# Kernel tuning notes

Measured on AMD Instinct MI355X. Metric: run time of the kernel, lower is better.

## Reference

```python
import jax, jax.numpy as jnp
import numpy as np

# FermiNet-style ansatz (Ansatz_fb) constants
N_U, N_D = 10, 10
N_E = N_U + N_D          # 20 electrons
N_A = 4                  # atoms
N_DET = 16
N_FB = 3
N_SV, N_PV = 256, 32
N_SV_OUT = 3 * N_SV + 2 * N_PV   # 832
N_B = 2048               # MCMC walkers (batch)
N_S_IN = 4 * N_A         # 16
N_P_IN = 4
D0 = 3 * N_S_IN + 2 * N_P_IN     # 56, input dim of first single-stream layer


def _lin(key, fan_in, shape):
    lim = 1.0 / np.sqrt(fan_in)
    return jax.random.uniform(key, shape, jnp.float32, -lim, lim)


def setup_inputs() -> dict:
    key = jax.random.key(0)
    ks = jax.random.split(key, 20)
    a = jnp.array([[0.0, 0.0, 0.0], [0.0, 0.0, 2.0], [2.0, 0.0, 0.0], [0.0, 2.0, 0.0]], jnp.float32)
    return {
        "r": jax.random.normal(ks[0], (N_B, N_E, 3), jnp.float32),
        "a": a,
        # single-stream layers: layer0 (D0->N_SV) then N_FB residual layers (N_SV_OUT->N_SV)
        "s_w0": _lin(ks[1], D0, (D0, N_SV)), "s_b0": _lin(ks[2], D0, (N_SV,)),
        "s_w": _lin(ks[3], N_SV_OUT, (N_FB, N_SV_OUT, N_SV)), "s_b": _lin(ks[4], N_SV_OUT, (N_FB, N_SV)),
        # pair-stream layers: layer0 (4->N_PV) then N_FB residual layers (N_PV->N_PV)
        "p_w0": _lin(ks[5], N_P_IN, (N_P_IN, N_PV)), "p_b0": _lin(ks[6], N_P_IN, (N_PV,)),
        "p_w": _lin(ks[7], N_PV, (N_FB, N_PV, N_PV)), "p_b": _lin(ks[8], N_PV, (N_FB, N_PV)),
        "vu_w": _lin(ks[9], N_SV_OUT, (N_SV_OUT, N_SV)), "vu_b": _lin(ks[10], N_SV_OUT, (N_SV,)),
        "vd_w": _lin(ks[11], N_SV_OUT, (N_SV_OUT, N_SV)), "vd_b": _lin(ks[12], N_SV_OUT, (N_SV,)),
        "wu_w": _lin(ks[13], N_SV, (N_SV, N_U * N_DET)), "wu_b": _lin(ks[14], N_SV, (N_U * N_DET,)),
        "wd_w": _lin(ks[15], N_SV, (N_SV, N_D * N_DET)), "wd_b": _lin(ks[16], N_SV, (N_D * N_DET,)),
        "wf_w": _lin(ks[17], N_DET, (N_DET, 1)),
    }


def fb_block(s_v, p_v):
    # s_v: [b, n_e, ds]; p_v: [b, n_e, n_e, dp]
    m_u = jnp.broadcast_to(s_v[:, :N_U].mean(1, keepdims=True), s_v.shape)  # tile mean over electrons
    m_d = jnp.broadcast_to(s_v[:, N_U:].mean(1, keepdims=True), s_v.shape)
    p_u = p_v[:, :N_U].mean(1)  # [b, n_e, dp]
    p_d = p_v[:, N_U:].mean(1)
    return jnp.concatenate([s_v, m_u, m_d, p_u, p_d], -1)


def reference(r, a, s_w0, s_b0, s_w, s_b, p_w0, p_b0, p_w, p_b, vu_w, vu_b, vd_w, vd_b, wu_w, wu_b, wd_w, wd_b, wf_w):
    n_b = r.shape[0]
    ra = r[:, :, None, :] - a[None, None]                      # [b, n_e, n_a, 3]
    ra_len = jnp.linalg.norm(ra, axis=-1, keepdims=True)
    rr = r[:, None, :, :] - r[:, :, None, :]                   # [b, n_e, n_e, 3]
    eye = jnp.eye(N_E, dtype=r.dtype)[None, :, :, None]
    rr_len = jnp.linalg.norm(rr + eye, axis=-1, keepdims=True)  # avoid 0 on diagonal
    s_v = jnp.concatenate([ra, ra_len], -1).reshape(n_b, N_E, -1)  # [b, n_e, 4*n_a]
    p_v = jnp.concatenate([rr, rr_len], -1)                        # [b, n_e, n_e, 4]

    blk = fb_block(s_v, p_v)
    s_v = jnp.tanh(blk @ s_w0 + s_b0)          # layer 0: no residual
    p_v = jnp.tanh(p_v @ p_w0 + p_b0)
    blk = fb_block(s_v, p_v)
    for i in range(N_FB):                       # residual layers
        s_v = jnp.tanh(blk @ s_w[i] + s_b[i]) + s_v
        p_v = jnp.tanh(p_v @ p_w[i] + p_b[i]) + p_v
        blk = fb_block(s_v, p_v)

    s_u = jnp.tanh(blk[:, :N_U] @ vu_w + vu_b)  # [b, n_u, n_sv]
    s_d = jnp.tanh(blk[:, N_U:] @ vd_w + vd_b)
    # chunk(n_det, dim=-1) then cat on new dim 1 == reshape+transpose
    w_u = (s_u @ wu_w + wu_b).reshape(n_b, N_U, N_DET, N_U).transpose(0, 2, 1, 3)  # [b, det, n_u, n_u]
    w_d = (s_d @ wd_w + wd_b).reshape(n_b, N_D, N_DET, N_D).transpose(0, 2, 1, 3)

    exp_u = jnp.exp(-jnp.linalg.norm(ra[:, :N_U], axis=-1)).sum(-1)  # [b, n_u]
    exp_d = jnp.exp(-jnp.linalg.norm(ra[:, N_U:], axis=-1)).sum(-1)
    orb_u = w_u * exp_u[:, None, :, None]
    orb_d = w_d * exp_d[:, None, :, None]

    # n_u, n_d > 1 -> det_one_e == 1, use slogdet path
    s_u_sgn, l_u = jnp.linalg.slogdet(orb_u)
    s_d_sgn, l_d = jnp.linalg.slogdet(orb_d)
    logdet = l_u + l_d                                       # [b, n_det]
    maxlogdet = jnp.max(logdet, axis=-1, keepdims=True)       # n_det > 1
    det = (s_u_sgn * s_d_sgn) * jnp.exp(logdet - maxlogdet)
    psi_ish = (det @ wf_w)[..., 0]                            # [b]
    log_psi = jnp.log(jnp.abs(psi_ish)) + maxlogdet[..., 0]
    return log_psi
```

## Files before the change

kernel.cpp:

```cpp
#include <hip/hip_runtime.h>
#include <math.h>


namespace {

constexpr float SQRT3 = 1.7320508075688772f;

__global__ __launch_bounds__(256, 2) void ansatz_fused(
    const float* __restrict__ r,
    const float* __restrict__ a_g,
    const float* __restrict__ s_w0,
    const float* __restrict__ s_b0,
    const float* __restrict__ s_w,
    const float* __restrict__ s_b,
    const float* __restrict__ p_w0,
    const float* __restrict__ p_b0,
    const float* __restrict__ p_w,
    const float* __restrict__ p_b,
    const float* __restrict__ vu_w, const float* __restrict__ vu_b,
    const float* __restrict__ vd_w, const float* __restrict__ vd_b,
    const float* __restrict__ wu_w, const float* __restrict__ wu_b,
    const float* __restrict__ wd_w, const float* __restrict__ wd_b,
    const float* __restrict__ wf_w,
    float* __restrict__ out)
{
  const int b = blockIdx.x;
  const int tid = threadIdx.x;

  __shared__ float svT[256 * 20];
  __shared__ float pvbuf[20 * 20 * 32];
  __shared__ float mu[256], md[256];
  __shared__ float puT[32 * 20], pdT[32 * 20];
  __shared__ float sinT[16 * 20];
  __shared__ float rl[20][3];
  __shared__ float apos[4][3];
  __shared__ float expv[20];
  __shared__ float lu_s[32], sg_s[32];

  if (tid < 60) (&rl[0][0])[tid] = r[b * 60 + tid];
  if (tid >= 64 && tid < 76) (&apos[0][0])[tid - 64] = a_g[tid - 64];
  __syncthreads();

  for (int t = tid; t < 320; t += 256) {
    int k = t / 20, e = t % 20;
    int at = k >> 2, comp = k & 3;
    float dx = rl[e][0] - apos[at][0];
    float dy = rl[e][1] - apos[at][1];
    float dz = rl[e][2] - apos[at][2];
    float v;
    if (comp == 0) v = dx;
    else if (comp == 1) v = dy;
    else if (comp == 2) v = dz;
    else v = sqrtf(dx * dx + dy * dy + dz * dz);
    sinT[k * 20 + e] = v;
  }
  for (int t = tid; t < 160; t += 256) {
    int half = t / 80, rem = t % 80, c = rem / 20, j = rem % 20;
    float s = 0.f;
    for (int i = half * 10; i < half * 10 + 10; ++i) {
      if (c < 3) {
        s += rl[j][c] - rl[i][c];
      } else if (i == j) {
        s += SQRT3;
      } else {
        float dx = rl[j][0] - rl[i][0], dy = rl[j][1] - rl[i][1], dz = rl[j][2] - rl[i][2];
        s += sqrtf(dx * dx + dy * dy + dz * dz);
      }
    }
    (half ? pdT : puT)[c * 20 + j] = s * 0.1f;
  }
  __syncthreads();

  if (tid < 20) {
    float s = 0.f;
    for (int at = 0; at < 4; ++at) s += expf(-sinT[(at * 4 + 3) * 20 + tid]);
    expv[tid] = s;
  }
  if (tid < 32) {
    int k = tid & 15, half = tid >> 4;
    float s = 0.f;
    for (int e = half * 10; e < half * 10 + 10; ++e) s += sinT[k * 20 + e];
    (half ? md : mu)[k] = s * 0.1f;
  }
  __syncthreads();

  {
    const int j = tid;
    float accm = s_b0[j];
#pragma unroll
    for (int k = 0; k < 16; ++k)
      accm += mu[k] * s_w0[(16 + k) * 256 + j] + md[k] * s_w0[(32 + k) * 256 + j];
    float sv0[20];
#pragma unroll
    for (int e = 0; e < 20; ++e) {
      float acc = accm;
#pragma unroll
      for (int k = 0; k < 16; ++k) acc += sinT[k * 20 + e] * s_w0[k * 256 + j];
#pragma unroll
      for (int c = 0; c < 4; ++c)
        acc += puT[c * 20 + e] * s_w0[(48 + c) * 256 + j] +
               pdT[c * 20 + e] * s_w0[(52 + c) * 256 + j];
      sv0[e] = tanhf(acc);
    }
#pragma unroll
    for (int e = 0; e < 20; ++e) svT[j * 20 + e] = sv0[e];
  }
  {
    const int c = tid & 31;
    float pw0c[4];
#pragma unroll
    for (int k = 0; k < 4; ++k) pw0c[k] = p_w0[k * 32 + c];
    const float pb0c = p_b0[c];
    for (int s = 0; s < 50; ++s) {
      int o = tid + 256 * s;
      int i = o / 640, rem = o % 640, j = rem >> 5;
      float dx = rl[j][0] - rl[i][0], dy = rl[j][1] - rl[i][1], dz = rl[j][2] - rl[i][2];
      float len = (i == j) ? SQRT3 : sqrtf(dx * dx + dy * dy + dz * dz);
      pvbuf[o] = tanhf(pb0c + dx * pw0c[0] + dy * pw0c[1] + dz * pw0c[2] + len * pw0c[3]);
    }
  }
  __syncthreads();

  for (int l = 0; l < 4; ++l) {
    {
      const int k = tid;
      float su_ = 0.f, sd_ = 0.f;
#pragma unroll
      for (int e = 0; e < 10; ++e) su_ += svT[k * 20 + e];
#pragma unroll
      for (int e = 10; e < 20; ++e) sd_ += svT[k * 20 + e];
      mu[k] = su_ * 0.1f;
      md[k] = sd_ * 0.1f;
    }
#pragma unroll
    for (int t5 = 0; t5 < 5; ++t5) {
      int t = tid + 256 * t5;
      int half = t / 640, rem = t % 640, j = rem >> 5, c = rem & 31;
      float s = 0.f;
      for (int i = half * 10; i < half * 10 + 10; ++i) s += pvbuf[(i * 20 + j) * 32 + c];
      (half ? pdT : puT)[c * 20 + j] = s * 0.1f;
    }
    __syncthreads();
    if (l == 3) break;

    const float* W = s_w + l * 832 * 256;
    const float* PW = p_w + l * 1024;

    const int j = tid;
    float sacc[20];
    {
      float accm = s_b[l * 256 + j];
#pragma unroll 4
      for (int k = 0; k < 256; ++k)
        accm += mu[k] * W[(256 + k) * 256 + j] + md[k] * W[(512 + k) * 256 + j];
#pragma unroll
      for (int e = 0; e < 20; ++e) sacc[e] = accm;
#pragma unroll 2
      for (int k = 0; k < 256; ++k) {
        float wk = W[k * 256 + j];
        const float* row = &svT[k * 20];
#pragma unroll
        for (int e = 0; e < 20; ++e) sacc[e] += row[e] * wk;
      }
#pragma unroll 2
      for (int c = 0; c < 32; ++c) {
        float wuc = W[(768 + c) * 256 + j], wdc = W[(800 + c) * 256 + j];
        const float* ru_ = &puT[c * 20];
        const float* rd_ = &pdT[c * 20];
#pragma unroll
        for (int e = 0; e < 20; ++e) sacc[e] += ru_[e] * wuc + rd_[e] * wdc;
      }
#pragma unroll
      for (int e = 0; e < 20; ++e) sacc[e] = tanhf(sacc[e]);
    }
    __syncthreads();
#pragma unroll
    for (int e = 0; e < 20; ++e) svT[j * 20 + e] += sacc[e];

    {
      const int c = tid & 31;
      float pwc[32];
#pragma unroll
      for (int k = 0; k < 32; ++k) pwc[k] = PW[k * 32 + c];
      const float pbc = p_b[l * 32 + c];
      float pacc[25];
#pragma unroll
      for (int s = 0; s < 25; ++s) {
        int o = tid + 256 * s;
        const float* row = &pvbuf[o & ~31];
        float acc = pbc;
#pragma unroll
        for (int k = 0; k < 32; ++k) acc += row[k] * pwc[k];
        pacc[s] = tanhf(acc);
      }
      __syncthreads();
#pragma unroll
      for (int s = 0; s < 25; ++s) pvbuf[tid + 256 * s] += pacc[s];
#pragma unroll
      for (int s = 25; s < 50; ++s) {
        int o = tid + 256 * s;
        const float* row = &pvbuf[o & ~31];
        float acc = pbc;
#pragma unroll
        for (int k = 0; k < 32; ++k) acc += row[k] * pwc[k];
        pacc[s - 25] = tanhf(acc);
      }
      __syncthreads();
#pragma unroll
      for (int s = 25; s < 50; ++s) pvbuf[tid + 256 * s] += pacc[s - 25];
    }
    __syncthreads();
  }

  float* suT = pvbuf;
  float* sdT = pvbuf + 256 * 12;
  float* orb = pvbuf + 2 * 256 * 12;
#pragma unroll
  for (int s = 0; s < 2; ++s) {
    const float* W = s ? vd_w : vu_w;
    const float* Bv = s ? vd_b : vu_b;
    float* dst = s ? sdT : suT;
    const int e0 = s * 10;
    const int j = tid;
    float accm = Bv[j];
#pragma unroll 4
    for (int k = 0; k < 256; ++k)
      accm += mu[k] * W[(256 + k) * 256 + j] + md[k] * W[(512 + k) * 256 + j];
    float acc[10];
#pragma unroll
    for (int e = 0; e < 10; ++e) acc[e] = accm;
#pragma unroll 2
    for (int k = 0; k < 256; ++k) {
      float wk = W[k * 256 + j];
      const float* row = &svT[k * 20 + e0];
#pragma unroll
      for (int e = 0; e < 10; ++e) acc[e] += row[e] * wk;
    }
#pragma unroll 2
    for (int c = 0; c < 32; ++c) {
      float wuc = W[(768 + c) * 256 + j], wdc = W[(800 + c) * 256 + j];
#pragma unroll
      for (int e = 0; e < 10; ++e)
        acc[e] += puT[c * 20 + e0 + e] * wuc + pdT[c * 20 + e0 + e] * wdc;
    }
#pragma unroll
    for (int e = 0; e < 10; ++e) dst[j * 12 + e] = tanhf(acc[e]);
  }
  __syncthreads();

  for (int t = tid; t < 320; t += 256) {
    const int mat = t / 160, col = t % 160;
    const float* W = mat ? wd_w : wu_w;
    const float* Bv = mat ? wd_b : wu_b;
    const float* src = mat ? sdT : suT;
    float acc[10];
    const float bb = Bv[col];
#pragma unroll
    for (int e = 0; e < 10; ++e) acc[e] = bb;
#pragma unroll 2
    for (int k = 0; k < 256; ++k) {
      float wk = W[k * 160 + col];
      const float* row = &src[k * 12];
#pragma unroll
      for (int e = 0; e < 10; ++e) acc[e] += row[e] * wk;
    }
    const int d = col / 10, jo = col % 10;
#pragma unroll
    for (int e = 0; e < 10; ++e)
      orb[(mat * 16 + d) * 100 + e * 10 + jo] = acc[e] * expv[mat * 10 + e];
  }
  __syncthreads();

  if (tid < 32) {
    float* M = orb + tid * 100;
    float ldet = 0.f, sg = 1.f;
    for (int c = 0; c < 10; ++c) {
      int p = c;
      float mx = fabsf(M[c * 10 + c]);
      for (int rr = c + 1; rr < 10; ++rr) {
        float v = fabsf(M[rr * 10 + c]);
        if (v > mx) { mx = v; p = rr; }
      }
      if (p != c) {
        sg = -sg;
        for (int cc = c; cc < 10; ++cc) {
          float tmp = M[c * 10 + cc];
          M[c * 10 + cc] = M[p * 10 + cc];
          M[p * 10 + cc] = tmp;
        }
      }
      float piv = M[c * 10 + c];
      if (piv < 0.f) sg = -sg;
      ldet += logf(fabsf(piv));
      float inv = 1.f / piv;
      for (int rr = c + 1; rr < 10; ++rr) {
        float f = M[rr * 10 + c] * inv;
        for (int cc = c + 1; cc < 10; ++cc) M[rr * 10 + cc] -= f * M[c * 10 + cc];
      }
    }
    lu_s[tid] = ldet;
    sg_s[tid] = sg;
  }
  __syncthreads();

  if (tid == 0) {
    float mx = -1e30f;
    float l[16], sgn[16];
#pragma unroll
    for (int d = 0; d < 16; ++d) {
      l[d] = lu_s[d] + lu_s[16 + d];
      sgn[d] = sg_s[d] * sg_s[16 + d];
      mx = fmaxf(mx, l[d]);
    }
    float psi = 0.f;
#pragma unroll
    for (int d = 0; d < 16; ++d) psi += sgn[d] * expf(l[d] - mx) * wf_w[d];
    out[b] = logf(fabsf(psi)) + mx;
  }
}

}

extern "C" void kernel_launch(void* const* d_in, const int* in_sizes, int n_in,
                              void* d_out, int out_size, void* d_ws, size_t ws_size,
                              hipStream_t stream) {
  const float* r = (const float*)d_in[0];
  const float* a = (const float*)d_in[1];
  const float* s_w0 = (const float*)d_in[2];
  const float* s_b0 = (const float*)d_in[3];
  const float* s_w = (const float*)d_in[4];
  const float* s_b = (const float*)d_in[5];
  const float* p_w0 = (const float*)d_in[6];
  const float* p_b0 = (const float*)d_in[7];
  const float* p_w = (const float*)d_in[8];
  const float* p_b = (const float*)d_in[9];
  const float* vu_w = (const float*)d_in[10];
  const float* vu_b = (const float*)d_in[11];
  const float* vd_w = (const float*)d_in[12];
  const float* vd_b = (const float*)d_in[13];
  const float* wu_w = (const float*)d_in[14];
  const float* wu_b = (const float*)d_in[15];
  const float* wd_w = (const float*)d_in[16];
  const float* wd_b = (const float*)d_in[17];
  const float* wf_w = (const float*)d_in[18];

  const int nb = in_sizes[0] / 60;
  ansatz_fused<<<dim3(nb), dim3(256), 0, stream>>>(
      r, a, s_w0, s_b0, s_w, s_b, p_w0, p_b0, p_w, p_b,
      vu_w, vu_b, vd_w, vd_b, wu_w, wu_b, wd_w, wd_b, wf_w,
      (float*)d_out);
}
```

Measured before the change: 2.086 ms.

## Software-pipeline weight loads, vectorize LDS reads, fast tanh, in-place pair update

Replaces tanhf/expf with fast exp+rcp approximations and register-prefetches weight columns in double-buffered groups of 8 for the single-stream, v and w GEMVs. LDS rows are now read with float4 vector loads, and the sinT table is replaced by on-the-fly features from positions plus a small length table. The pair-stream residual update now runs in place in one pass instead of two staged halves with extra barriers, and orbitals reuse svT storage. The intent is to cut global-load latency, LDS instruction count, transcendental cost and synchronisation. The trade-offs are higher register pressure and slightly lower tanh accuracy.

```diff
diff --git a/kernel.cpp b/kernel.cpp
--- a/kernel.cpp
+++ b/kernel.cpp
@@ -5,6 +5,11 @@
 namespace {
 
 constexpr float SQRT3 = 1.7320508075688772f;
+
+__device__ __forceinline__ float tanh_fast(float x) {
+  float e = __expf(2.f * x);
+  return 1.f - 2.f * __builtin_amdgcn_rcpf(e + 1.f);
+}
 
 __global__ __launch_bounds__(256, 2) void ansatz_fused(
     const float* __restrict__ r,
@@ -27,11 +32,11 @@
   const int b = blockIdx.x;
   const int tid = threadIdx.x;
 
-  __shared__ float svT[256 * 20];
-  __shared__ float pvbuf[20 * 20 * 32];
-  __shared__ float mu[256], md[256];
-  __shared__ float puT[32 * 20], pdT[32 * 20];
-  __shared__ float sinT[16 * 20];
+  __shared__ __align__(16) float svT[256 * 20];
+  __shared__ __align__(16) float pv[12800];
+  __shared__ __align__(16) float mu[256], md[256];
+  __shared__ __align__(16) float puT[640], pdT[640];
+  __shared__ float lenT[80];
   __shared__ float rl[20][3];
   __shared__ float apos[4][3];
   __shared__ float expv[20];
@@ -41,51 +46,53 @@
   if (tid >= 64 && tid < 76) (&apos[0][0])[tid - 64] = a_g[tid - 64];
   __syncthreads();
 
-  for (int t = tid; t < 320; t += 256) {
-    int k = t / 20, e = t % 20;
-    int at = k >> 2, comp = k & 3;
+  if (tid < 80) {
+    int at = tid / 20, e = tid % 20;
     float dx = rl[e][0] - apos[at][0];
     float dy = rl[e][1] - apos[at][1];
     float dz = rl[e][2] - apos[at][2];
-    float v;
-    if (comp == 0) v = dx;
-    else if (comp == 1) v = dy;
-    else if (comp == 2) v = dz;
-    else v = sqrtf(dx * dx + dy * dy + dz * dz);
-    sinT[k * 20 + e] = v;
-  }
-  for (int t = tid; t < 160; t += 256) {
-    int half = t / 80, rem = t % 80, c = rem / 20, j = rem % 20;
+    lenT[tid] = sqrtf(dx * dx + dy * dy + dz * dz);
+  }
+  if (tid < 160) {
+    int half = tid / 80, rem = tid % 80, c = rem / 20, j2 = rem % 20;
     float s = 0.f;
     for (int i = half * 10; i < half * 10 + 10; ++i) {
       if (c < 3) {
-        s += rl[j][c] - rl[i][c];
-      } else if (i == j) {
+        s += rl[j2][c] - rl[i][c];
+      } else if (i == j2) {
         s += SQRT3;
       } else {
-        float dx = rl[j][0] - rl[i][0], dy = rl[j][1] - rl[i][1], dz = rl[j][2] - rl[i][2];
+        float dx = rl[j2][0] - rl[i][0], dy = rl[j2][1] - rl[i][1], dz = rl[j2][2] - rl[i][2];
         s += sqrtf(dx * dx + dy * dy + dz * dz);
       }
     }
-    (half ? pdT : puT)[c * 20 + j] = s * 0.1f;
+    (half ? pdT : puT)[c * 20 + j2] = s * 0.1f;
   }
   __syncthreads();
 
   if (tid < 20) {
     float s = 0.f;
-    for (int at = 0; at < 4; ++at) s += expf(-sinT[(at * 4 + 3) * 20 + tid]);
+#pragma unroll
+    for (int at = 0; at < 4; ++at) s += __expf(-lenT[at * 20 + tid]);
     expv[tid] = s;
   }
   if (tid < 32) {
     int k = tid & 15, half = tid >> 4;
+    int at = k >> 2, comp = k & 3;
     float s = 0.f;
-    for (int e = half * 10; e < half * 10 + 10; ++e) s += sinT[k * 20 + e];
+    for (int e = half * 10; e < half * 10 + 10; ++e)
+      s += (comp < 3) ? (rl[e][comp] - apos[at][comp]) : lenT[at * 20 + e];
     (half ? md : mu)[k] = s * 0.1f;
   }
   __syncthreads();
 
   {
     const int j = tid;
+    float w0s[16], wpp[8];
+#pragma unroll
+    for (int k = 0; k < 16; ++k) w0s[k] = s_w0[k * 256 + j];
+#pragma unroll
+    for (int c = 0; c < 8; ++c) wpp[c] = s_w0[(48 + c) * 256 + j];
     float accm = s_b0[j];
 #pragma unroll
     for (int k = 0; k < 16; ++k)
@@ -95,12 +102,16 @@
     for (int e = 0; e < 20; ++e) {
       float acc = accm;
 #pragma unroll
-      for (int k = 0; k < 16; ++k) acc += sinT[k * 20 + e] * s_w0[k * 256 + j];
+      for (int at = 0; at < 4; ++at) {
+        acc += (rl[e][0] - apos[at][0]) * w0s[at * 4 + 0];
+        acc += (rl[e][1] - apos[at][1]) * w0s[at * 4 + 1];
+        acc += (rl[e][2] - apos[at][2]) * w0s[at * 4 + 2];
+        acc += lenT[at * 20 + e] * w0s[at * 4 + 3];
+      }
 #pragma unroll
       for (int c = 0; c < 4; ++c)
-        acc += puT[c * 20 + e] * s_w0[(48 + c) * 256 + j] +
-               pdT[c * 20 + e] * s_w0[(52 + c) * 256 + j];
-      sv0[e] = tanhf(acc);
+        acc += puT[c * 20 + e] * wpp[c] + pdT[c * 20 + e] * wpp[4 + c];
+      sv0[e] = tanh_fast(acc);
     }
 #pragma unroll
     for (int e = 0; e < 20; ++e) svT[j * 20 + e] = sv0[e];
@@ -113,69 +124,149 @@
     const float pb0c = p_b0[c];
     for (int s = 0; s < 50; ++s) {
       int o = tid + 256 * s;
-      int i = o / 640, rem = o % 640, j = rem >> 5;
-      float dx = rl[j][0] - rl[i][0], dy = rl[j][1] - rl[i][1], dz = rl[j][2] - rl[i][2];
-      float len = (i == j) ? SQRT3 : sqrtf(dx * dx + dy * dy + dz * dz);
-      pvbuf[o] = tanhf(pb0c + dx * pw0c[0] + dy * pw0c[1] + dz * pw0c[2] + len * pw0c[3]);
+      int ij = o >> 5, i = ij / 20, j2 = ij % 20;
+      float dx = rl[j2][0] - rl[i][0], dy = rl[j2][1] - rl[i][1], dz = rl[j2][2] - rl[i][2];
+      float len = (i == j2) ? SQRT3 : sqrtf(dx * dx + dy * dy + dz * dz);
+      pv[o] = tanh_fast(pb0c + dx * pw0c[0] + dy * pw0c[1] + dz * pw0c[2] + len * pw0c[3]);
     }
   }
   __syncthreads();
 
   for (int l = 0; l < 4; ++l) {
     {
-      const int k = tid;
-      float su_ = 0.f, sd_ = 0.f;
-#pragma unroll
-      for (int e = 0; e < 10; ++e) su_ += svT[k * 20 + e];
-#pragma unroll
-      for (int e = 10; e < 20; ++e) sd_ += svT[k * 20 + e];
-      mu[k] = su_ * 0.1f;
-      md[k] = sd_ * 0.1f;
+      const float4* svr = (const float4*)&svT[tid * 20];
+      float4 a0 = svr[0], a1 = svr[1], a2 = svr[2], a3 = svr[3], a4 = svr[4];
+      mu[tid] = (a0.x + a0.y + a0.z + a0.w + a1.x + a1.y + a1.z + a1.w + a2.x + a2.y) * 0.1f;
+      md[tid] = (a2.z + a2.w + a3.x + a3.y + a3.z + a3.w + a4.x + a4.y + a4.z + a4.w) * 0.1f;
     }
 #pragma unroll
     for (int t5 = 0; t5 < 5; ++t5) {
       int t = tid + 256 * t5;
-      int half = t / 640, rem = t % 640, j = rem >> 5, c = rem & 31;
+      int half = t / 640, rem = t % 640, j2 = rem >> 5, c = rem & 31;
+      int base = half * 6400 + j2 * 32 + c;
       float s = 0.f;
-      for (int i = half * 10; i < half * 10 + 10; ++i) s += pvbuf[(i * 20 + j) * 32 + c];
-      (half ? pdT : puT)[c * 20 + j] = s * 0.1f;
+#pragma unroll
+      for (int i = 0; i < 10; ++i) s += pv[base + i * 640];
+      (half ? pdT : puT)[c * 20 + j2] = s * 0.1f;
     }
     __syncthreads();
     if (l == 3) break;
 
-    const float* W = s_w + l * 832 * 256;
+    const float* Wj = s_w + l * 832 * 256 + tid;
     const float* PW = p_w + l * 1024;
 
-    const int j = tid;
     float sacc[20];
+#pragma unroll
+    for (int e = 0; e < 20; ++e) sacc[e] = 0.f;
+    float m0 = 0.f, m1 = 0.f, m2 = 0.f, m3 = 0.f;
     {
-      float accm = s_b[l * 256 + j];
-#pragma unroll 4
-      for (int k = 0; k < 256; ++k)
-        accm += mu[k] * W[(256 + k) * 256 + j] + md[k] * W[(512 + k) * 256 + j];
-#pragma unroll
-      for (int e = 0; e < 20; ++e) sacc[e] = accm;
-#pragma unroll 2
-      for (int k = 0; k < 256; ++k) {
-        float wk = W[k * 256 + j];
-        const float* row = &svT[k * 20];
-#pragma unroll
-        for (int e = 0; e < 20; ++e) sacc[e] += row[e] * wk;
-      }
-#pragma unroll 2
-      for (int c = 0; c < 32; ++c) {
-        float wuc = W[(768 + c) * 256 + j], wdc = W[(800 + c) * 256 + j];
-        const float* ru_ = &puT[c * 20];
-        const float* rd_ = &pdT[c * 20];
-#pragma unroll
-        for (int e = 0; e < 20; ++e) sacc[e] += ru_[e] * wuc + rd_[e] * wdc;
-      }
-#pragma unroll
-      for (int e = 0; e < 20; ++e) sacc[e] = tanhf(sacc[e]);
+      float As[8], Au[8], Ad[8], Bs[8], Bu[8], Bd[8];
+#pragma unroll
+      for (int i = 0; i < 8; ++i) {
+        As[i] = Wj[i * 256]; Au[i] = Wj[(256 + i) * 256]; Ad[i] = Wj[(512 + i) * 256];
+      }
+      for (int k0 = 0; k0 < 256; k0 += 16) {
+#pragma unroll
+        for (int i = 0; i < 8; ++i) {
+          Bs[i] = Wj[(k0 + 8 + i) * 256];
+          Bu[i] = Wj[(264 + k0 + i) * 256];
+          Bd[i] = Wj[(520 + k0 + i) * 256];
+        }
+        {
+          float muv[8], mdv[8];
+          *(float4*)&muv[0] = *(const float4*)&mu[k0];
+          *(float4*)&muv[4] = *(const float4*)&mu[k0 + 4];
+          *(float4*)&mdv[0] = *(const float4*)&md[k0];
+          *(float4*)&mdv[4] = *(const float4*)&md[k0 + 4];
+#pragma unroll
+          for (int i = 0; i < 8; i += 2) {
+            m0 = fmaf(muv[i], Au[i], m0);     m1 = fmaf(mdv[i], Ad[i], m1);
+            m2 = fmaf(muv[i + 1], Au[i + 1], m2); m3 = fmaf(mdv[i + 1], Ad[i + 1], m3);
+          }
+#pragma unroll
+          for (int i = 0; i < 8; ++i) {
+            float rr[20];
+            const float4* rw = (const float4*)&svT[(k0 + i) * 20];
+            *(float4*)&rr[0] = rw[0]; *(float4*)&rr[4] = rw[1]; *(float4*)&rr[8] = rw[2];
+            *(float4*)&rr[12] = rw[3]; *(float4*)&rr[16] = rw[4];
+            float w = As[i];
+#pragma unroll
+            for (int e = 0; e < 20; ++e) sacc[e] = fmaf(rr[e], w, sacc[e]);
+          }
+        }
+        if (k0 + 16 < 256) {
+#pragma unroll
+          for (int i = 0; i < 8; ++i) {
+            As[i] = Wj[(k0 + 16 + i) * 256];
+            Au[i] = Wj[(272 + k0 + i) * 256];
+            Ad[i] = Wj[(528 + k0 + i) * 256];
+          }
+        }
+        {
+          float muv[8], mdv[8];
+          *(float4*)&muv[0] = *(const float4*)&mu[k0 + 8];
+          *(float4*)&muv[4] = *(const float4*)&mu[k0 + 12];
+          *(float4*)&mdv[0] = *(const float4*)&md[k0 + 8];
+          *(float4*)&mdv[4] = *(const float4*)&md[k0 + 12];
+#pragma unroll
+          for (int i = 0; i < 8; i += 2) {
+            m0 = fmaf(muv[i], Bu[i], m0);     m1 = fmaf(mdv[i], Bd[i], m1);
+            m2 = fmaf(muv[i + 1], Bu[i + 1], m2); m3 = fmaf(mdv[i + 1], Bd[i + 1], m3);
+          }
+#pragma unroll
+          for (int i = 0; i < 8; ++i) {
+            float rr[20];
+            const float4* rw = (const float4*)&svT[(k0 + 8 + i) * 20];
+            *(float4*)&rr[0] = rw[0]; *(float4*)&rr[4] = rw[1]; *(float4*)&rr[8] = rw[2];
+            *(float4*)&rr[12] = rw[3]; *(float4*)&rr[16] = rw[4];
+            float w = Bs[i];
+#pragma unroll
+            for (int e = 0; e < 20; ++e) sacc[e] = fmaf(rr[e], w, sacc[e]);
+          }
+        }
+      }
+      float AU[4], AD[4], BU[4], BD[4];
+#pragma unroll
+      for (int i = 0; i < 4; ++i) { AU[i] = Wj[(768 + i) * 256]; AD[i] = Wj[(800 + i) * 256]; }
+      for (int c0 = 0; c0 < 32; c0 += 8) {
+#pragma unroll
+        for (int i = 0; i < 4; ++i) { BU[i] = Wj[(772 + c0 + i) * 256]; BD[i] = Wj[(804 + c0 + i) * 256]; }
+#pragma unroll
+        for (int i = 0; i < 4; ++i) {
+          float ru[20], rd[20];
+          const float4* pu4 = (const float4*)&puT[(c0 + i) * 20];
+          const float4* pd4 = (const float4*)&pdT[(c0 + i) * 20];
+          *(float4*)&ru[0] = pu4[0]; *(float4*)&ru[4] = pu4[1]; *(float4*)&ru[8] = pu4[2];
+          *(float4*)&ru[12] = pu4[3]; *(float4*)&ru[16] = pu4[4];
+          *(float4*)&rd[0] = pd4[0]; *(float4*)&rd[4] = pd4[1]; *(float4*)&rd[8] = pd4[2];
+          *(float4*)&rd[12] = pd4[3]; *(float4*)&rd[16] = pd4[4];
+#pragma unroll
+          for (int e = 0; e < 20; ++e) sacc[e] = fmaf(rd[e], AD[i], fmaf(ru[e], AU[i], sacc[e]));
+        }
+        if (c0 + 8 < 32) {
+#pragma unroll
+          for (int i = 0; i < 4; ++i) { AU[i] = Wj[(776 + c0 + i) * 256]; AD[i] = Wj[(808 + c0 + i) * 256]; }
+        }
+#pragma unroll
+        for (int i = 0; i < 4; ++i) {
+          float ru[20], rd[20];
+          const float4* pu4 = (const float4*)&puT[(c0 + 4 + i) * 20];
+          const float4* pd4 = (const float4*)&pdT[(c0 + 4 + i) * 20];
+          *(float4*)&ru[0] = pu4[0]; *(float4*)&ru[4] = pu4[1]; *(float4*)&ru[8] = pu4[2];
+          *(float4*)&ru[12] = pu4[3]; *(float4*)&ru[16] = pu4[4];
+          *(float4*)&rd[0] = pd4[0]; *(float4*)&rd[4] = pd4[1]; *(float4*)&rd[8] = pd4[2];
+          *(float4*)&rd[12] = pd4[3]; *(float4*)&rd[16] = pd4[4];
+#pragma unroll
+          for (int e = 0; e < 20; ++e) sacc[e] = fmaf(rd[e], BD[i], fmaf(ru[e], BU[i], sacc[e]));
+        }
+      }
+      float accm = s_b[l * 256 + tid] + ((m0 + m1) + (m2 + m3));
+#pragma unroll
+      for (int e = 0; e < 20; ++e) sacc[e] = tanh_fast(sacc[e] + accm);
     }
     __syncthreads();
 #pragma unroll
-    for (int e = 0; e < 20; ++e) svT[j * 20 + e] += sacc[e];
+    for (int e = 0; e < 20; ++e) svT[tid * 20 + e] += sacc[e];
 
     {
       const int c = tid & 31;
@@ -183,91 +274,164 @@
 #pragma unroll
       for (int k = 0; k < 32; ++k) pwc[k] = PW[k * 32 + c];
       const float pbc = p_b[l * 32 + c];
-      float pacc[25];
-#pragma unroll
-      for (int s = 0; s < 25; ++s) {
+      for (int s = 0; s < 50; ++s) {
         int o = tid + 256 * s;
-        const float* row = &pvbuf[o & ~31];
+        const float4* q4 = (const float4*)&pv[(o >> 5) << 5];
+        float row[32];
+#pragma unroll
+        for (int q = 0; q < 8; ++q) *(float4*)&row[4 * q] = q4[q];
         float acc = pbc;
 #pragma unroll
-        for (int k = 0; k < 32; ++k) acc += row[k] * pwc[k];
-        pacc[s] = tanhf(acc);
-      }
-      __syncthreads();
-#pragma unroll
-      for (int s = 0; s < 25; ++s) pvbuf[tid + 256 * s] += pacc[s];
-#pragma unroll
-      for (int s = 25; s < 50; ++s) {
-        int o = tid + 256 * s;
-        const float* row = &pvbuf[o & ~31];
-        float acc = pbc;
-#pragma unroll
-        for (int k = 0; k < 32; ++k) acc += row[k] * pwc[k];
-        pacc[s - 25] = tanhf(acc);
-      }
-      __syncthreads();
-#pragma unroll
-      for (int s = 25; s < 50; ++s) pvbuf[tid + 256 * s] += pacc[s - 25];
+        for (int k = 0; k < 32; ++k) acc = fmaf(row[k], pwc[k], acc);
+        pv[o] = row[c] + tanh_fast(acc);
+      }
     }
     __syncthreads();
   }
 
-  float* suT = pvbuf;
-  float* sdT = pvbuf + 256 * 12;
-  float* orb = pvbuf + 2 * 256 * 12;
-#pragma unroll
-  for (int s = 0; s < 2; ++s) {
-    const float* W = s ? vd_w : vu_w;
-    const float* Bv = s ? vd_b : vu_b;
-    float* dst = s ? sdT : suT;
-    const int e0 = s * 10;
+  float* suT = pv;
+  float* sdT = pv + 256 * 12;
+  {
     const int j = tid;
-    float accm = Bv[j];
-#pragma unroll 4
-    for (int k = 0; k < 256; ++k)
-      accm += mu[k] * W[(256 + k) * 256 + j] + md[k] * W[(512 + k) * 256 + j];
-    float acc[10];
-#pragma unroll
-    for (int e = 0; e < 10; ++e) acc[e] = accm;
-#pragma unroll 2
-    for (int k = 0; k < 256; ++k) {
-      float wk = W[k * 256 + j];
-      const float* row = &svT[k * 20 + e0];
-#pragma unroll
-      for (int e = 0; e < 10; ++e) acc[e] += row[e] * wk;
-    }
-#pragma unroll 2
-    for (int c = 0; c < 32; ++c) {
-      float wuc = W[(768 + c) * 256 + j], wdc = W[(800 + c) * 256 + j];
-#pragma unroll
-      for (int e = 0; e < 10; ++e)
-        acc[e] += puT[c * 20 + e0 + e] * wuc + pdT[c * 20 + e0 + e] * wdc;
-    }
-#pragma unroll
-    for (int e = 0; e < 10; ++e) dst[j * 12 + e] = tanhf(acc[e]);
-  }
-  __syncthreads();
-
+#pragma unroll
+    for (int sS = 0; sS < 2; ++sS) {
+      const float* Wj = (sS ? vd_w : vu_w) + j;
+      const float* Bv = sS ? vd_b : vu_b;
+      float* dst = sS ? sdT : suT;
+      const int e0 = sS * 10;
+      float acc[10];
+#pragma unroll
+      for (int e = 0; e < 10; ++e) acc[e] = 0.f;
+      float m0 = 0.f, m1 = 0.f, m2 = 0.f, m3 = 0.f;
+      float As[8], Au[8], Ad[8], Bs[8], Bu[8], Bd[8];
+#pragma unroll
+      for (int i = 0; i < 8; ++i) {
+        As[i] = Wj[i * 256]; Au[i] = Wj[(256 + i) * 256]; Ad[i] = Wj[(512 + i) * 256];
+      }
+      for (int k0 = 0; k0 < 256; k0 += 16) {
+#pragma unroll
+        for (int i = 0; i < 8; ++i) {
+          Bs[i] = Wj[(k0 + 8 + i) * 256];
+          Bu[i] = Wj[(264 + k0 + i) * 256];
+          Bd[i] = Wj[(520 + k0 + i) * 256];
+        }
+        {
+          float muv[8], mdv[8];
+          *(float4*)&muv[0] = *(const float4*)&mu[k0];
+          *(float4*)&muv[4] = *(const float4*)&mu[k0 + 4];
+          *(float4*)&mdv[0] = *(const float4*)&md[k0];
+          *(float4*)&mdv[4] = *(const float4*)&md[k0 + 4];
+#pragma unroll
+          for (int i = 0; i < 8; i += 2) {
+            m0 = fmaf(muv[i], Au[i], m0);     m1 = fmaf(mdv[i], Ad[i], m1);
+            m2 = fmaf(muv[i + 1], Au[i + 1], m2); m3 = fmaf(mdv[i + 1], Ad[i + 1], m3);
+          }
+#pragma unroll
+          for (int i = 0; i < 8; ++i) {
+            float rr[20];
+            const float4* rw = (const float4*)&svT[(k0 + i) * 20];
+            *(float4*)&rr[0] = rw[0]; *(float4*)&rr[4] = rw[1]; *(float4*)&rr[8] = rw[2];
+            *(float4*)&rr[12] = rw[3]; *(float4*)&rr[16] = rw[4];
+            float w = As[i];
+#pragma unroll
+            for (int e = 0; e < 10; ++e) acc[e] = fmaf(rr[e0 + e], w, acc[e]);
+          }
+        }
+        if (k0 + 16 < 256) {
+#pragma unroll
+          for (int i = 0; i < 8; ++i) {
+            As[i] = Wj[(k0 + 16 + i) * 256];
+            Au[i] = Wj[(272 + k0 + i) * 256];
+            Ad[i] = Wj[(528 + k0 + i) * 256];
+          }
+        }
+        {
+          float muv[8], mdv[8];
+          *(float4*)&muv[0] = *(const float4*)&mu[k0 + 8];
+          *(float4*)&muv[4] = *(const float4*)&mu[k0 + 12];
+          *(float4*)&mdv[0] = *(const float4*)&md[k0 + 8];
+          *(float4*)&mdv[4] = *(const float4*)&md[k0 + 12];
+#pragma unroll
+          for (int i = 0; i < 8; i += 2) {
+            m0 = fmaf(muv[i], Bu[i], m0);     m1 = fmaf(mdv[i], Bd[i], m1);
+            m2 = fmaf(muv[i + 1], Bu[i + 1], m2); m3 = fmaf(mdv[i + 1], Bd[i + 1], m3);
+          }
+#pragma unroll
+          for (int i = 0; i < 8; ++i) {
+            float rr[20];
+            const float4* rw = (const float4*)&svT[(k0 + 8 + i) * 20];
+            *(float4*)&rr[0] = rw[0]; *(float4*)&rr[4] = rw[1]; *(float4*)&rr[8] = rw[2];
+            *(float4*)&rr[12] = rw[3]; *(float4*)&rr[16] = rw[4];
+            float w = Bs[i];
+#pragma unroll
+            for (int e = 0; e < 10; ++e) acc[e] = fmaf(rr[e0 + e], w, acc[e]);
+          }
+        }
+      }
+      float AU[4], AD[4];
+      for (int c0 = 0; c0 < 32; c0 += 4) {
+#pragma unroll
+        for (int i = 0; i < 4; ++i) { AU[i] = Wj[(768 + c0 + i) * 256]; AD[i] = Wj[(800 + c0 + i) * 256]; }
+#pragma unroll
+        for (int i = 0; i < 4; ++i) {
+#pragma unroll
+          for (int e = 0; e < 10; ++e)
+            acc[e] = fmaf(pdT[(c0 + i) * 20 + e0 + e], AD[i],
+                     fmaf(puT[(c0 + i) * 20 + e0 + e], AU[i], acc[e]));
+        }
+      }
+      float accm = Bv[j] + ((m0 + m1) + (m2 + m3));
+#pragma unroll
+      for (int e = 0; e < 10; ++e) dst[j * 12 + e] = tanh_fast(acc[e] + accm);
+    }
+  }
+  __syncthreads();
+
+  float* orb = svT;
   for (int t = tid; t < 320; t += 256) {
     const int mat = t / 160, col = t % 160;
-    const float* W = mat ? wd_w : wu_w;
+    const float* Wc = (mat ? wd_w : wu_w) + col;
     const float* Bv = mat ? wd_b : wu_b;
     const float* src = mat ? sdT : suT;
     float acc[10];
+#pragma unroll
+    for (int e = 0; e < 10; ++e) acc[e] = 0.f;
+    float wA[8], wB[8];
+#pragma unroll
+    for (int i = 0; i < 8; ++i) wA[i] = Wc[i * 160];
+    for (int k0 = 0; k0 < 256; k0 += 16) {
+#pragma unroll
+      for (int i = 0; i < 8; ++i) wB[i] = Wc[(k0 + 8 + i) * 160];
+#pragma unroll
+      for (int i = 0; i < 8; ++i) {
+        float rr[12];
+        *(float4*)&rr[0] = *(const float4*)&src[(k0 + i) * 12];
+        *(float4*)&rr[4] = *(const float4*)&src[(k0 + i) * 12 + 4];
+        *(float2*)&rr[8] = *(const float2*)&src[(k0 + i) * 12 + 8];
+        float w = wA[i];
+#pragma unroll
+        for (int e = 0; e < 10; ++e) acc[e] = fmaf(rr[e], w, acc[e]);
+      }
+      if (k0 + 16 < 256) {
+#pragma unroll
+        for (int i = 0; i < 8; ++i) wA[i] = Wc[(k0 + 16 + i) * 160];
+      }
+#pragma unroll
+      for (int i = 0; i < 8; ++i) {
+        float rr[12];
+        *(float4*)&rr[0] = *(const float4*)&src[(k0 + 8 + i) * 12];
+        *(float4*)&rr[4] = *(const float4*)&src[(k0 + 8 + i) * 12 + 4];
+        *(float2*)&rr[8] = *(const float2*)&src[(k0 + 8 + i) * 12 + 8];
+        float w = wB[i];
+#pragma unroll
+        for (int e = 0; e < 10; ++e) acc[e] = fmaf(rr[e], w, acc[e]);
+      }
+    }
     const float bb = Bv[col];
-#pragma unroll
-    for (int e = 0; e < 10; ++e) acc[e] = bb;
-#pragma unroll 2
-    for (int k = 0; k < 256; ++k) {
-      float wk = W[k * 160 + col];
-      const float* row = &src[k * 12];
-#pragma unroll
-      for (int e = 0; e < 10; ++e) acc[e] += row[e] * wk;
-    }
     const int d = col / 10, jo = col % 10;
 #pragma unroll
     for (int e = 0; e < 10; ++e)
-      orb[(mat * 16 + d) * 100 + e * 10 + jo] = acc[e] * expv[mat * 10 + e];
+      orb[(mat * 16 + d) * 100 + e * 10 + jo] = (acc[e] + bb) * expv[mat * 10 + e];
   }
   __syncthreads();
 
@@ -314,7 +478,7 @@
     }
     float psi = 0.f;
 #pragma unroll
-    for (int d = 0; d < 16; ++d) psi += sgn[d] * expf(l[d] - mx) * wf_w[d];
+    for (int d = 0; d < 16; ++d) psi += sgn[d] * __expf(l[d] - mx) * wf_w[d];
     out[b] = logf(fabsf(psi)) + mx;
   }
 }
```

Result: slower. 3.336 ms (+59.9%).

## Move per-walker activations to global workspace, fast tanh, in-place pair update

Applied to the files above, without the earlier changes.

Moves the per-walker single-stream activation rows and electron means out of shared memory into a per-block global workspace, keeping the residual state in registers. This shrinks shared memory so more blocks fit per CU (launch bounds raised to 3). It also swaps tanhf/expf for fast exp-and-reciprocal versions, vectorises the row reads with float4 and a merged 320-row loop, and updates the pair stream in place without double buffering. The cost is global/L2 traffic for activations, lower-precision tanh, and an in-place pair update that relies on every thread in a 32-wide row group reading that row before any lane writes it back.

```diff
diff --git a/kernel.cpp b/kernel.cpp
--- a/kernel.cpp
+++ b/kernel.cpp
@@ -6,7 +6,27 @@
 
 constexpr float SQRT3 = 1.7320508075688772f;
 
-__global__ __launch_bounds__(256, 2) void ansatz_fused(
+__device__ __forceinline__ float tanh_fast(float x) {
+  float e = __expf(2.f * x);
+  return 1.f - 2.f * __builtin_amdgcn_rcpf(e + 1.f);
+}
+
+__device__ __forceinline__ void fma20(float* a, const float4 r0, const float4 r1,
+                                      const float4 r2, const float4 r3, const float4 r4,
+                                      const float w) {
+  a[0] = fmaf(r0.x, w, a[0]);   a[1] = fmaf(r0.y, w, a[1]);
+  a[2] = fmaf(r0.z, w, a[2]);   a[3] = fmaf(r0.w, w, a[3]);
+  a[4] = fmaf(r1.x, w, a[4]);   a[5] = fmaf(r1.y, w, a[5]);
+  a[6] = fmaf(r1.z, w, a[6]);   a[7] = fmaf(r1.w, w, a[7]);
+  a[8] = fmaf(r2.x, w, a[8]);   a[9] = fmaf(r2.y, w, a[9]);
+  a[10] = fmaf(r2.z, w, a[10]); a[11] = fmaf(r2.w, w, a[11]);
+  a[12] = fmaf(r3.x, w, a[12]); a[13] = fmaf(r3.y, w, a[13]);
+  a[14] = fmaf(r3.z, w, a[14]); a[15] = fmaf(r3.w, w, a[15]);
+  a[16] = fmaf(r4.x, w, a[16]); a[17] = fmaf(r4.y, w, a[17]);
+  a[18] = fmaf(r4.z, w, a[18]); a[19] = fmaf(r4.w, w, a[19]);
+}
+
+__global__ __launch_bounds__(256, 3) void ansatz_fused(
     const float* __restrict__ r,
     const float* __restrict__ a_g,
     const float* __restrict__ s_w0,
@@ -22,88 +42,111 @@
     const float* __restrict__ wu_w, const float* __restrict__ wu_b,
     const float* __restrict__ wd_w, const float* __restrict__ wd_b,
     const float* __restrict__ wf_w,
+    float* __restrict__ ws,
     float* __restrict__ out)
 {
   const int b = blockIdx.x;
   const int tid = threadIdx.x;
 
-  __shared__ float svT[256 * 20];
-  __shared__ float pvbuf[20 * 20 * 32];
-  __shared__ float mu[256], md[256];
-  __shared__ float puT[32 * 20], pdT[32 * 20];
-  __shared__ float sinT[16 * 20];
+  float* gw = ws + (size_t)b * 12032;
+  float* rows  = gw;
+  float* gmu   = gw + 6400;
+  float* gmd   = gw + 6656;
+  float* rows2 = gw + 6912;
+
+  __shared__ __align__(16) float pv[12800];
   __shared__ float rl[20][3];
   __shared__ float apos[4][3];
+  __shared__ float lenT[80];
   __shared__ float expv[20];
-  __shared__ float lu_s[32], sg_s[32];
+  __shared__ float l0mu[16], l0md[16];
+  __shared__ float l0pu[80], l0pd[80];
 
   if (tid < 60) (&rl[0][0])[tid] = r[b * 60 + tid];
   if (tid >= 64 && tid < 76) (&apos[0][0])[tid - 64] = a_g[tid - 64];
   __syncthreads();
 
-  for (int t = tid; t < 320; t += 256) {
-    int k = t / 20, e = t % 20;
-    int at = k >> 2, comp = k & 3;
+  if (tid < 80) {
+    int at = tid / 20, e = tid % 20;
     float dx = rl[e][0] - apos[at][0];
     float dy = rl[e][1] - apos[at][1];
     float dz = rl[e][2] - apos[at][2];
-    float v;
-    if (comp == 0) v = dx;
-    else if (comp == 1) v = dy;
-    else if (comp == 2) v = dz;
-    else v = sqrtf(dx * dx + dy * dy + dz * dz);
-    sinT[k * 20 + e] = v;
-  }
-  for (int t = tid; t < 160; t += 256) {
-    int half = t / 80, rem = t % 80, c = rem / 20, j = rem % 20;
+    lenT[tid] = sqrtf(dx * dx + dy * dy + dz * dz);
+  }
+  if (tid < 160) {
+    int half = tid / 80, rem = tid % 80, c = rem / 20, j2 = rem % 20;
     float s = 0.f;
     for (int i = half * 10; i < half * 10 + 10; ++i) {
       if (c < 3) {
-        s += rl[j][c] - rl[i][c];
-      } else if (i == j) {
+        s += rl[j2][c] - rl[i][c];
+      } else if (i == j2) {
         s += SQRT3;
       } else {
-        float dx = rl[j][0] - rl[i][0], dy = rl[j][1] - rl[i][1], dz = rl[j][2] - rl[i][2];
+        float dx = rl[j2][0] - rl[i][0], dy = rl[j2][1] - rl[i][1], dz = rl[j2][2] - rl[i][2];
         s += sqrtf(dx * dx + dy * dy + dz * dz);
       }
     }
-    (half ? pdT : puT)[c * 20 + j] = s * 0.1f;
+    (half ? l0pd : l0pu)[c * 20 + j2] = s * 0.1f;
   }
   __syncthreads();
 
   if (tid < 20) {
     float s = 0.f;
-    for (int at = 0; at < 4; ++at) s += expf(-sinT[(at * 4 + 3) * 20 + tid]);
+#pragma unroll
+    for (int at = 0; at < 4; ++at) s += __expf(-lenT[at * 20 + tid]);
     expv[tid] = s;
   }
   if (tid < 32) {
     int k = tid & 15, half = tid >> 4;
+    int at = k >> 2, comp = k & 3;
     float s = 0.f;
-    for (int e = half * 10; e < half * 10 + 10; ++e) s += sinT[k * 20 + e];
-    (half ? md : mu)[k] = s * 0.1f;
-  }
-  __syncthreads();
+    for (int e = half * 10; e < half * 10 + 10; ++e)
+      s += (comp < 3) ? (rl[e][comp] - apos[at][comp]) : lenT[at * 20 + e];
+    (half ? l0md : l0mu)[k] = s * 0.1f;
+  }
+  __syncthreads();
+
+  float sv_reg[20];
 
   {
     const int j = tid;
+    float w0s[16], wpp[8];
+#pragma unroll
+    for (int k = 0; k < 16; ++k) w0s[k] = s_w0[k * 256 + j];
+#pragma unroll
+    for (int c = 0; c < 8; ++c) wpp[c] = s_w0[(48 + c) * 256 + j];
     float accm = s_b0[j];
 #pragma unroll
     for (int k = 0; k < 16; ++k)
-      accm += mu[k] * s_w0[(16 + k) * 256 + j] + md[k] * s_w0[(32 + k) * 256 + j];
-    float sv0[20];
+      accm += l0mu[k] * s_w0[(16 + k) * 256 + j] + l0md[k] * s_w0[(32 + k) * 256 + j];
 #pragma unroll
     for (int e = 0; e < 20; ++e) {
       float acc = accm;
 #pragma unroll
-      for (int k = 0; k < 16; ++k) acc += sinT[k * 20 + e] * s_w0[k * 256 + j];
+      for (int at = 0; at < 4; ++at) {
+        acc += (rl[e][0] - apos[at][0]) * w0s[at * 4 + 0];
+        acc += (rl[e][1] - apos[at][1]) * w0s[at * 4 + 1];
+        acc += (rl[e][2] - apos[at][2]) * w0s[at * 4 + 2];
+        acc += lenT[at * 20 + e] * w0s[at * 4 + 3];
+      }
 #pragma unroll
       for (int c = 0; c < 4; ++c)
-        acc += puT[c * 20 + e] * s_w0[(48 + c) * 256 + j] +
-               pdT[c * 20 + e] * s_w0[(52 + c) * 256 + j];
-      sv0[e] = tanhf(acc);
-    }
-#pragma unroll
-    for (int e = 0; e < 20; ++e) svT[j * 20 + e] = sv0[e];
+        acc += l0pu[c * 20 + e] * wpp[c] + l0pd[c * 20 + e] * wpp[4 + c];
+      sv_reg[e] = tanh_fast(acc);
+    }
+    float su_ = 0.f, sd_ = 0.f;
+#pragma unroll
+    for (int e = 0; e < 10; ++e) su_ += sv_reg[e];
+#pragma unroll
+    for (int e = 10; e < 20; ++e) sd_ += sv_reg[e];
+    gmu[tid] = su_ * 0.1f;
+    gmd[tid] = sd_ * 0.1f;
+    float4* rw = (float4*)&rows[tid * 20];
+    rw[0] = make_float4(sv_reg[0], sv_reg[1], sv_reg[2], sv_reg[3]);
+    rw[1] = make_float4(sv_reg[4], sv_reg[5], sv_reg[6], sv_reg[7]);
+    rw[2] = make_float4(sv_reg[8], sv_reg[9], sv_reg[10], sv_reg[11]);
+    rw[3] = make_float4(sv_reg[12], sv_reg[13], sv_reg[14], sv_reg[15]);
+    rw[4] = make_float4(sv_reg[16], sv_reg[17], sv_reg[18], sv_reg[19]);
   }
   {
     const int c = tid & 31;
@@ -113,161 +156,183 @@
     const float pb0c = p_b0[c];
     for (int s = 0; s < 50; ++s) {
       int o = tid + 256 * s;
-      int i = o / 640, rem = o % 640, j = rem >> 5;
-      float dx = rl[j][0] - rl[i][0], dy = rl[j][1] - rl[i][1], dz = rl[j][2] - rl[i][2];
-      float len = (i == j) ? SQRT3 : sqrtf(dx * dx + dy * dy + dz * dz);
-      pvbuf[o] = tanhf(pb0c + dx * pw0c[0] + dy * pw0c[1] + dz * pw0c[2] + len * pw0c[3]);
-    }
-  }
+      int ij = o >> 5, i = ij / 20, j2 = ij % 20;
+      float dx = rl[j2][0] - rl[i][0], dy = rl[j2][1] - rl[i][1], dz = rl[j2][2] - rl[i][2];
+      float len = (i == j2) ? SQRT3 : sqrtf(dx * dx + dy * dy + dz * dz);
+      pv[o] = tanh_fast(pb0c + dx * pw0c[0] + dy * pw0c[1] + dz * pw0c[2] + len * pw0c[3]);
+    }
+  }
+  __threadfence_block();
   __syncthreads();
 
   for (int l = 0; l < 4; ++l) {
-    {
-      const int k = tid;
-      float su_ = 0.f, sd_ = 0.f;
-#pragma unroll
-      for (int e = 0; e < 10; ++e) su_ += svT[k * 20 + e];
-#pragma unroll
-      for (int e = 10; e < 20; ++e) sd_ += svT[k * 20 + e];
-      mu[k] = su_ * 0.1f;
-      md[k] = sd_ * 0.1f;
-    }
 #pragma unroll
     for (int t5 = 0; t5 < 5; ++t5) {
       int t = tid + 256 * t5;
-      int half = t / 640, rem = t % 640, j = rem >> 5, c = rem & 31;
+      int half = t / 640, rem = t % 640, j2 = rem >> 5, c = rem & 31;
+      int base = half * 6400 + j2 * 32 + c;
       float s = 0.f;
-      for (int i = half * 10; i < half * 10 + 10; ++i) s += pvbuf[(i * 20 + j) * 32 + c];
-      (half ? pdT : puT)[c * 20 + j] = s * 0.1f;
-    }
+#pragma unroll
+      for (int i = 0; i < 10; ++i) s += pv[base + i * 640];
+      rows[(256 + half * 32 + c) * 20 + j2] = s * 0.1f;
+    }
+    __threadfence_block();
     __syncthreads();
     if (l == 3) break;
 
-    const float* W = s_w + l * 832 * 256;
-    const float* PW = p_w + l * 1024;
-
-    const int j = tid;
+    const float* Wj = s_w + l * 832 * 256 + tid;
+
+    float m0 = 0.f, m1 = 0.f, m2 = 0.f, m3 = 0.f;
+    for (int k = 0; k < 256; k += 4) {
+      int mo = k;
+      asm volatile("" : "+v"(mo));
+      float4 u = *(const float4*)&gmu[mo];
+      float4 d = *(const float4*)&gmd[mo];
+      m0 = fmaf(u.x, Wj[(256 + k) * 256], m0);
+      m1 = fmaf(u.y, Wj[(257 + k) * 256], m1);
+      m2 = fmaf(u.z, Wj[(258 + k) * 256], m2);
+      m3 = fmaf(u.w, Wj[(259 + k) * 256], m3);
+      m0 = fmaf(d.x, Wj[(512 + k) * 256], m0);
+      m1 = fmaf(d.y, Wj[(513 + k) * 256], m1);
+      m2 = fmaf(d.z, Wj[(514 + k) * 256], m2);
+      m3 = fmaf(d.w, Wj[(515 + k) * 256], m3);
+    }
+
     float sacc[20];
+#pragma unroll
+    for (int e = 0; e < 20; ++e) sacc[e] = 0.f;
+    for (int k = 0; k < 320; ++k) {
+      int ro = k * 20;
+      asm volatile("" : "+v"(ro));
+      const float4* rp = (const float4*)(rows + ro);
+      float4 r0 = rp[0], r1 = rp[1], r2 = rp[2], r3 = rp[3], r4 = rp[4];
+      int wr = k + ((k >> 8) << 9);
+      float w = Wj[wr * 256];
+      fma20(sacc, r0, r1, r2, r3, r4, w);
+    }
+    __syncthreads();
+
+    float accm = s_b[l * 256 + tid] + ((m0 + m1) + (m2 + m3));
+    float su_ = 0.f, sd_ = 0.f;
+#pragma unroll
+    for (int e = 0; e < 20; ++e) {
+      sv_reg[e] += tanh_fast(sacc[e] + accm);
+      if (e < 10) su_ += sv_reg[e]; else sd_ += sv_reg[e];
+    }
+    gmu[tid] = su_ * 0.1f;
+    gmd[tid] = sd_ * 0.1f;
     {
-      float accm = s_b[l * 256 + j];
-#pragma unroll 4
-      for (int k = 0; k < 256; ++k)
-        accm += mu[k] * W[(256 + k) * 256 + j] + md[k] * W[(512 + k) * 256 + j];
-#pragma unroll
-      for (int e = 0; e < 20; ++e) sacc[e] = accm;
-#pragma unroll 2
-      for (int k = 0; k < 256; ++k) {
-        float wk = W[k * 256 + j];
-        const float* row = &svT[k * 20];
-#pragma unroll
-        for (int e = 0; e < 20; ++e) sacc[e] += row[e] * wk;
-      }
-#pragma unroll 2
-      for (int c = 0; c < 32; ++c) {
-        float wuc = W[(768 + c) * 256 + j], wdc = W[(800 + c) * 256 + j];
-        const float* ru_ = &puT[c * 20];
-        const float* rd_ = &pdT[c * 20];
-#pragma unroll
-        for (int e = 0; e < 20; ++e) sacc[e] += ru_[e] * wuc + rd_[e] * wdc;
-      }
-#pragma unroll
-      for (int e = 0; e < 20; ++e) sacc[e] = tanhf(sacc[e]);
-    }
-    __syncthreads();
-#pragma unroll
-    for (int e = 0; e < 20; ++e) svT[j * 20 + e] += sacc[e];
+      float4* rw = (float4*)&rows[tid * 20];
+      rw[0] = make_float4(sv_reg[0], sv_reg[1], sv_reg[2], sv_reg[3]);
+      rw[1] = make_float4(sv_reg[4], sv_reg[5], sv_reg[6], sv_reg[7]);
+      rw[2] = make_float4(sv_reg[8], sv_reg[9], sv_reg[10], sv_reg[11]);
+      rw[3] = make_float4(sv_reg[12], sv_reg[13], sv_reg[14], sv_reg[15]);
+      rw[4] = make_float4(sv_reg[16], sv_reg[17], sv_reg[18], sv_reg[19]);
+    }
 
     {
+      const float* PW = p_w + l * 1024;
       const int c = tid & 31;
       float pwc[32];
 #pragma unroll
       for (int k = 0; k < 32; ++k) pwc[k] = PW[k * 32 + c];
       const float pbc = p_b[l * 32 + c];
-      float pacc[25];
-#pragma unroll
-      for (int s = 0; s < 25; ++s) {
+      for (int s = 0; s < 50; ++s) {
         int o = tid + 256 * s;
-        const float* row = &pvbuf[o & ~31];
+        const float4* q4 = (const float4*)&pv[(o >> 5) << 5];
+        float row[32];
+#pragma unroll
+        for (int q = 0; q < 8; ++q) *(float4*)&row[4 * q] = q4[q];
         float acc = pbc;
 #pragma unroll
-        for (int k = 0; k < 32; ++k) acc += row[k] * pwc[k];
-        pacc[s] = tanhf(acc);
-      }
-      __syncthreads();
-#pragma unroll
-      for (int s = 0; s < 25; ++s) pvbuf[tid + 256 * s] += pacc[s];
-#pragma unroll
-      for (int s = 25; s < 50; ++s) {
-        int o = tid + 256 * s;
-        const float* row = &pvbuf[o & ~31];
-        float acc = pbc;
-#pragma unroll
-        for (int k = 0; k < 32; ++k) acc += row[k] * pwc[k];
-        pacc[s - 25] = tanhf(acc);
-      }
-      __syncthreads();
-#pragma unroll
-      for (int s = 25; s < 50; ++s) pvbuf[tid + 256 * s] += pacc[s - 25];
-    }
+        for (int k = 0; k < 32; ++k) acc = fmaf(row[k], pwc[k], acc);
+        pv[o] = row[c] + tanh_fast(acc);
+      }
+    }
+    __threadfence_block();
     __syncthreads();
   }
 
-  float* suT = pvbuf;
-  float* sdT = pvbuf + 256 * 12;
-  float* orb = pvbuf + 2 * 256 * 12;
-#pragma unroll
-  for (int s = 0; s < 2; ++s) {
-    const float* W = s ? vd_w : vu_w;
-    const float* Bv = s ? vd_b : vu_b;
-    float* dst = s ? sdT : suT;
-    const int e0 = s * 10;
-    const int j = tid;
-    float accm = Bv[j];
-#pragma unroll 4
-    for (int k = 0; k < 256; ++k)
-      accm += mu[k] * W[(256 + k) * 256 + j] + md[k] * W[(512 + k) * 256 + j];
-    float acc[10];
-#pragma unroll
-    for (int e = 0; e < 10; ++e) acc[e] = accm;
-#pragma unroll 2
-    for (int k = 0; k < 256; ++k) {
-      float wk = W[k * 256 + j];
-      const float* row = &svT[k * 20 + e0];
-#pragma unroll
-      for (int e = 0; e < 10; ++e) acc[e] += row[e] * wk;
-    }
-#pragma unroll 2
-    for (int c = 0; c < 32; ++c) {
-      float wuc = W[(768 + c) * 256 + j], wdc = W[(800 + c) * 256 + j];
-#pragma unroll
-      for (int e = 0; e < 10; ++e)
-        acc[e] += puT[c * 20 + e0 + e] * wuc + pdT[c * 20 + e0 + e] * wdc;
-    }
-#pragma unroll
-    for (int e = 0; e < 10; ++e) dst[j * 12 + e] = tanhf(acc[e]);
-  }
-  __syncthreads();
-
+  {
+    const float* Wu = vu_w + tid;
+    const float* Wd = vd_w + tid;
+    float au[10], ad[10];
+#pragma unroll
+    for (int e = 0; e < 10; ++e) { au[e] = 0.f; ad[e] = 0.f; }
+    for (int k = 0; k < 320; ++k) {
+      int ro = k * 20;
+      asm volatile("" : "+v"(ro));
+      const float4* rp = (const float4*)(rows + ro);
+      float4 r0 = rp[0], r1 = rp[1], r2 = rp[2], r3 = rp[3], r4 = rp[4];
+      int wr = k + ((k >> 8) << 9);
+      float wu = Wu[wr * 256], wd = Wd[wr * 256];
+      au[0] = fmaf(r0.x, wu, au[0]); au[1] = fmaf(r0.y, wu, au[1]);
+      au[2] = fmaf(r0.z, wu, au[2]); au[3] = fmaf(r0.w, wu, au[3]);
+      au[4] = fmaf(r1.x, wu, au[4]); au[5] = fmaf(r1.y, wu, au[5]);
+      au[6] = fmaf(r1.z, wu, au[6]); au[7] = fmaf(r1.w, wu, au[7]);
+      au[8] = fmaf(r2.x, wu, au[8]); au[9] = fmaf(r2.y, wu, au[9]);
+      ad[0] = fmaf(r2.z, wd, ad[0]); ad[1] = fmaf(r2.w, wd, ad[1]);
+      ad[2] = fmaf(r3.x, wd, ad[2]); ad[3] = fmaf(r3.y, wd, ad[3]);
+      ad[4] = fmaf(r3.z, wd, ad[4]); ad[5] = fmaf(r3.w, wd, ad[5]);
+      ad[6] = fmaf(r4.x, wd, ad[6]); ad[7] = fmaf(r4.y, wd, ad[7]);
+      ad[8] = fmaf(r4.z, wd, ad[8]); ad[9] = fmaf(r4.w, wd, ad[9]);
+    }
+    float a0 = 0.f, a1 = 0.f, b0 = 0.f, b1 = 0.f;
+    for (int k = 0; k < 256; k += 2) {
+      int mo = k;
+      asm volatile("" : "+v"(mo));
+      float2 u = *(const float2*)&gmu[mo];
+      float2 d = *(const float2*)&gmd[mo];
+      a0 = fmaf(u.x, Wu[(256 + k) * 256], a0);
+      a1 = fmaf(u.y, Wu[(257 + k) * 256], a1);
+      a0 = fmaf(d.x, Wu[(512 + k) * 256], a0);
+      a1 = fmaf(d.y, Wu[(513 + k) * 256], a1);
+      b0 = fmaf(u.x, Wd[(256 + k) * 256], b0);
+      b1 = fmaf(u.y, Wd[(257 + k) * 256], b1);
+      b0 = fmaf(d.x, Wd[(512 + k) * 256], b0);
+      b1 = fmaf(d.y, Wd[(513 + k) * 256], b1);
+    }
+    const float accu = vu_b[tid] + a0 + a1;
+    const float accd = vd_b[tid] + b0 + b1;
+    float* dst = &rows2[tid * 20];
+#pragma unroll
+    for (int e = 0; e < 10; ++e) dst[e] = tanh_fast(au[e] + accu);
+#pragma unroll
+    for (int e = 0; e < 10; ++e) dst[10 + e] = tanh_fast(ad[e] + accd);
+  }
+  __threadfence_block();
+  __syncthreads();
+
+  float* orb = pv;
+  float* lu_s = pv + 3200;
+  float* sg_s = pv + 3232;
   for (int t = tid; t < 320; t += 256) {
     const int mat = t / 160, col = t % 160;
-    const float* W = mat ? wd_w : wu_w;
-    const float* Bv = mat ? wd_b : wu_b;
-    const float* src = mat ? sdT : suT;
+    const float* Wc = (mat ? wd_w : wu_w) + col;
+    const float bb = (mat ? wd_b : wu_b)[col];
     float acc[10];
-    const float bb = Bv[col];
-#pragma unroll
-    for (int e = 0; e < 10; ++e) acc[e] = bb;
-#pragma unroll 2
+#pragma unroll
+    for (int e = 0; e < 10; ++e) acc[e] = 0.f;
     for (int k = 0; k < 256; ++k) {
-      float wk = W[k * 160 + col];
-      const float* row = &src[k * 12];
-#pragma unroll
-      for (int e = 0; e < 10; ++e) acc[e] += row[e] * wk;
+      int ro = k * 20 + mat * 10;
+      asm volatile("" : "+v"(ro));
+      const float* rp = rows2 + ro;
+      float2 q0 = *(const float2*)rp;
+      float2 q1 = *(const float2*)(rp + 2);
+      float2 q2 = *(const float2*)(rp + 4);
+      float2 q3 = *(const float2*)(rp + 6);
+      float2 q4 = *(const float2*)(rp + 8);
+      float w = Wc[k * 160];
+      acc[0] = fmaf(q0.x, w, acc[0]); acc[1] = fmaf(q0.y, w, acc[1]);
+      acc[2] = fmaf(q1.x, w, acc[2]); acc[3] = fmaf(q1.y, w, acc[3]);
+      acc[4] = fmaf(q2.x, w, acc[4]); acc[5] = fmaf(q2.y, w, acc[5]);
+      acc[6] = fmaf(q3.x, w, acc[6]); acc[7] = fmaf(q3.y, w, acc[7]);
+      acc[8] = fmaf(q4.x, w, acc[8]); acc[9] = fmaf(q4.y, w, acc[9]);
     }
     const int d = col / 10, jo = col % 10;
 #pragma unroll
     for (int e = 0; e < 10; ++e)
-      orb[(mat * 16 + d) * 100 + e * 10 + jo] = acc[e] * expv[mat * 10 + e];
+      orb[(mat * 16 + d) * 100 + e * 10 + jo] = (acc[e] + bb) * expv[mat * 10 + e];
   }
   __syncthreads();
 
@@ -314,7 +379,7 @@
     }
     float psi = 0.f;
 #pragma unroll
-    for (int d = 0; d < 16; ++d) psi += sgn[d] * expf(l[d] - mx) * wf_w[d];
+    for (int d = 0; d < 16; ++d) psi += sgn[d] * __expf(l[d] - mx) * wf_w[d];
     out[b] = logf(fabsf(psi)) + mx;
   }
 }
@@ -348,5 +413,5 @@
   ansatz_fused<<<dim3(nb), dim3(256), 0, stream>>>(
       r, a, s_w0, s_b0, s_w, s_b, p_w0, p_b0, p_w, p_b,
       vu_w, vu_b, vd_w, vd_b, wu_w, wu_b, wd_w, wd_b, wf_w,
-      (float*)d_out);
+      (float*)d_ws, (float*)d_out);
 }
```

New measurement: 4.096 ms. 1.96x slower.
